# Performance work log

Measured on AMD Instinct MI355X. Metric: run time of the kernel, lower is better.

Reference implementation:

```python
import jax, jax.numpy as jnp
import numpy as np

LN_EPS = 1e-5
DEG_EPS = 1e-12


def setup_inputs() -> dict:
    key = jax.random.key(0)
    k1, k2, k3, k4 = jax.random.split(key, 4)
    N, E, D = 100000, 1000000, 64
    x = jax.random.normal(k1, (N, D), dtype=jnp.float32)
    edge_index = jax.random.randint(k2, (2, E), 0, N, dtype=jnp.int64)
    edge_weight = jax.random.uniform(k3, (E,), dtype=jnp.float32)
    # xavier_uniform for Linear(D, D): bound = sqrt(6/(D+D))
    bound = float(np.sqrt(6.0 / (D + D)))
    W = jax.random.uniform(k4, (D, D), dtype=jnp.float32, minval=-bound, maxval=bound)
    b = jnp.zeros((D,), dtype=jnp.float32)
    ln_gamma = jnp.ones((D,), dtype=jnp.float32)
    ln_beta = jnp.zeros((D,), dtype=jnp.float32)
    return {"x": x, "edge_index": edge_index, "edge_weight": edge_weight,
            "W": W, "b": b, "ln_gamma": ln_gamma, "ln_beta": ln_beta}


def reference(x, edge_index, edge_weight, W, b, ln_gamma, ln_beta):
    N = x.shape[0]
    # --- add self loops with weight 1.0 ---
    diag = jnp.arange(N, dtype=edge_index.dtype)
    ei = jnp.concatenate([edge_index, jnp.stack([diag, diag], axis=0)], axis=1)
    ew = jnp.concatenate([edge_weight.astype(jnp.float32),
                          jnp.ones((N,), dtype=jnp.float32)], axis=0)
    row, col = ei[0], ei[1]
    # --- renormalized adjacency weights: D^{-1/2}(A+I)D^{-1/2} ---
    deg = jax.ops.segment_sum(ew, row, num_segments=N)  # [N]
    deg_inv_sqrt = (deg + DEG_EPS) ** -0.5
    nw = ew * deg_inv_sqrt[row] * deg_inv_sqrt[col]     # [E+N]
    # --- SpMM: gather, scale, segment-sum ---
    msg = x[col] * nw[:, None].astype(x.dtype)          # [E+N, D]
    h = jax.ops.segment_sum(msg, row, num_segments=N)   # [N, D]
    # --- linear + gelu (exact erf) + layernorm + residual ---
    y = h @ W.T + b
    y = jax.nn.gelu(y, approximate=False)
    mean = jnp.mean(y, axis=-1, keepdims=True)
    var = jnp.mean(jnp.square(y - mean), axis=-1, keepdims=True)
    y = (y - mean) * jax.lax.rsqrt(var + LN_EPS) * ln_gamma + ln_beta
    return y + x
```

## Files before the change

kernel.cpp:

```cpp
#include <hip/hip_runtime.h>
#include <math.h>

#define DEG_EPS 1e-12f
#define LN_EPS  1e-5f
#define BROWS   128
#define CAPA    1536
#define MAXBKT  1024
#define CHUNK   2048

typedef __attribute__((ext_vector_type(8))) short bf16x8;
typedef __attribute__((ext_vector_type(4))) float f32x4;

__device__ __forceinline__ short f2bf(float f) {
    unsigned u = __float_as_uint(f);
    u += 0x7FFF + ((u >> 16) & 1);
    return (short)(u >> 16);
}
__device__ __forceinline__ float bf_lo(unsigned u) { return __uint_as_float(u << 16); }
__device__ __forceinline__ float bf_hi(unsigned u) { return __uint_as_float(u & 0xFFFF0000u); }


__global__ __launch_bounds__(256) void k_prep(
    const int* __restrict__ rows, const int* __restrict__ cols,
    const float* __restrict__ ew,
    int* __restrict__ bktcnt, int2* __restrict__ bktbuf,
    const float* __restrict__ x, const float* __restrict__ W,
    unsigned short* __restrict__ xwb,
    int E, int N, int NBKT, int Ntiles, int cB)
{
    const int t = threadIdx.x;
    if ((int)blockIdx.x < cB) {
        __shared__ int hist[MAXBKT];
        __shared__ int base_s[MAXBKT];
        __shared__ int cur[MAXBKT];
        __shared__ int srow[CHUNK];
        const int e0 = blockIdx.x * CHUNK;
        const int tc = min(E - e0, CHUNK);

        for (int i = t; i < NBKT; i += 256) { hist[i] = 0; cur[i] = 0; }
        __syncthreads();
        for (int i = t; i < tc; i += 256) {
            int r = rows[e0 + i];
            srow[i] = r;
            atomicAdd(&hist[r >> 7], 1);
        }
        __syncthreads();
        for (int i = t; i < NBKT; i += 256) {
            int h = hist[i];
            base_s[i] = h ? atomicAdd(&bktcnt[i], h) : 0;
        }
        __syncthreads();
        for (int i = t; i < tc; i += 256) {
            int r = srow[i];
            int bkt = r >> 7;
            int slot = base_s[bkt] + atomicAdd(&cur[bkt], 1);
            if (slot < CAPA)
                bktbuf[(size_t)bkt * CAPA + slot] =
                    make_int2(((r & 127) << 17) | cols[e0 + i],
                              __float_as_int(ew[e0 + i]));
        }
    } else {
        const int lane = t & 63;
        const int m = lane & 15;
        const int q = lane >> 4;
        const int xwB = gridDim.x - cB;
        const int wave = (blockIdx.x - cB) * 4 + (t >> 6);
        const int nwv = xwB * 4;

        bf16x8 bfrag[4][2];
#pragma unroll
        for (int f = 0; f < 4; ++f)
#pragma unroll
            for (int s = 0; s < 2; ++s) {
                const float4* wp = (const float4*)(W + (f * 16 + m) * 64 + s * 32 + q * 8);
                float4 lo = wp[0], hi = wp[1];
                bf16x8 v;
                v[0] = f2bf(lo.x); v[1] = f2bf(lo.y); v[2] = f2bf(lo.z); v[3] = f2bf(lo.w);
                v[4] = f2bf(hi.x); v[5] = f2bf(hi.y); v[6] = f2bf(hi.z); v[7] = f2bf(hi.w);
                bfrag[f][s] = v;
            }

        for (int tt = wave; tt < Ntiles; tt += nwv) {
            int n0 = tt * 16;
            int nr = n0 + m; if (nr >= N) nr = N - 1;
            bf16x8 afrag[2];
#pragma unroll
            for (int s = 0; s < 2; ++s) {
                const float4* xp = (const float4*)(x + (size_t)nr * 64 + s * 32 + q * 8);
                float4 lo = xp[0], hi = xp[1];
                bf16x8 v;
                v[0] = f2bf(lo.x); v[1] = f2bf(lo.y); v[2] = f2bf(lo.z); v[3] = f2bf(lo.w);
                v[4] = f2bf(hi.x); v[5] = f2bf(hi.y); v[6] = f2bf(hi.z); v[7] = f2bf(hi.w);
                afrag[s] = v;
            }
#pragma unroll
            for (int f = 0; f < 4; ++f) {
                f32x4 acc = {0.f, 0.f, 0.f, 0.f};
                acc = __builtin_amdgcn_mfma_f32_16x16x32_bf16(afrag[0], bfrag[f][0], acc, 0, 0, 0);
                acc = __builtin_amdgcn_mfma_f32_16x16x32_bf16(afrag[1], bfrag[f][1], acc, 0, 0, 0);
#pragma unroll
                for (int r4 = 0; r4 < 4; ++r4) {
                    int node = n0 + q * 4 + r4;
                    if (node < N)
                        xwb[(size_t)node * 64 + f * 16 + m] = (unsigned short)f2bf(acc[r4]);
                }
            }
        }
    }
}

__global__ __launch_bounds__(256) void k_dis(
    const int* __restrict__ bktcnt, const int2* __restrict__ bktbuf,
    float* __restrict__ dis, int N)
{
    __shared__ unsigned lsum[BROWS];
    const int bkt = blockIdx.x, t = threadIdx.x;
    if (t < BROWS) lsum[t] = 0;
    __syncthreads();
    int nb = bktcnt[bkt];
    if (nb > CAPA) nb = CAPA;
    const int2* buf = bktbuf + (size_t)bkt * CAPA;
    for (int i = t; i < nb; i += 256) {
        int2 e = buf[i];
        atomicAdd(&lsum[(e.x >> 17) & 127],
                  __float2uint_rn(__int_as_float(e.y) * 16777216.0f));
    }
    __syncthreads();
    int r = bkt * BROWS + t;
    if (t < BROWS && r < N) {
        float deg = 1.0f + (float)lsum[t] * (1.0f / 16777216.0f);
        dis[r] = rsqrtf(deg + DEG_EPS);
    }
}

__global__ __launch_bounds__(512) void k_spmm_fused(
    const int* __restrict__ bktcnt, const int2* __restrict__ bktbuf,
    const float* __restrict__ dis, const uint2* __restrict__ xw4,
    const float* __restrict__ x, const float* __restrict__ bias,
    const float* __restrict__ gamma, const float* __restrict__ beta,
    float* __restrict__ out, int N)
{
    __shared__ int2  srt[CAPA];
    __shared__ int   cnt[BROWS], off[BROWS], cur[BROWS], sc[BROWS];
    __shared__ float sdis[BROWS];
    const int t = threadIdx.x;
    const int bkt = blockIdx.x;
    const int r0 = bkt * BROWS;

    if (t < BROWS) {
        cnt[t] = 0; cur[t] = 0;
        sdis[t] = (r0 + t < N) ? dis[r0 + t] : 1.0f;
    }
    __syncthreads();

    int nb = bktcnt[bkt];
    if (nb > CAPA) nb = CAPA;
    const int2* buf = bktbuf + (size_t)bkt * CAPA;

    int2 eb[3];
#pragma unroll
    for (int u = 0; u < 3; ++u) {
        int i = t + u * 512;
        eb[u] = (i < nb) ? buf[i] : make_int2(-1, 0);
    }
#pragma unroll
    for (int u = 0; u < 3; ++u)
        if (eb[u].x >= 0)
            atomicAdd(&cnt[(eb[u].x >> 17) & 127], 1);
    __syncthreads();

    int v = 0;
    if (t < BROWS) { v = cnt[t]; sc[t] = v; }
    __syncthreads();
    for (int o = 1; o < BROWS; o <<= 1) {
        int u2 = 0;
        if (t < BROWS && t >= o) u2 = sc[t - o];
        __syncthreads();
        if (t < BROWS) sc[t] += u2;
        __syncthreads();
    }
    if (t < BROWS) off[t] = sc[t] - v;
    __syncthreads();

#pragma unroll
    for (int u = 0; u < 3; ++u)
        if (eb[u].x >= 0) {
            int rl = (eb[u].x >> 17) & 127;
            int c  = eb[u].x & 0x1FFFF;
            float w = __int_as_float(eb[u].y) * sdis[rl] * dis[c];
            int pos = off[rl] + atomicAdd(&cur[rl], 1);
            srt[pos] = make_int2(c, __float_as_int(w));
        }
    __syncthreads();

    const int lane = t & 63, wv = t >> 6;
    const int k  = lane & 15;
    const int qh = lane >> 4;

    for (int i = 0; i < 16; ++i) {
        const int rl = wv * 16 + i;
        const int row = r0 + rl;
        if (row >= N) break;

        int rcnt = cnt[rl]; if (rcnt > 64) rcnt = 64;
        int rbase = off[rl];
        float s = sdis[rl];

        float a0 = 0.f, a1 = 0.f, a2 = 0.f, a3 = 0.f;
        if (qh == 0) {
            float s2 = s * s;
            uint2 vv = xw4[(size_t)row * 16 + k];
            a0 = bf_lo(vv.x) * s2; a1 = bf_hi(vv.x) * s2;
            a2 = bf_lo(vv.y) * s2; a3 = bf_hi(vv.y) * s2;
        }

        int c = 0; float w = 0.f;
        if (lane < rcnt) {
            int2 m = srt[rbase + lane];
            c = m.x;
            w = __int_as_float(m.y);
        }

        int tmax = (rcnt + 3) >> 2;
        int tt = 0;
        for (; tt + 2 <= tmax; tt += 2) {
            int j0 = 4 * tt + qh, j1 = j0 + 4;
            int   c0 = __shfl(c, j0, 64);
            float w0 = __shfl(w, j0, 64);
            int   c1 = __shfl(c, j1, 64);
            float w1 = __shfl(w, j1, 64);
            uint2 v0 = xw4[(size_t)c0 * 16 + k];
            uint2 v1 = xw4[(size_t)c1 * 16 + k];
            a0 = fmaf(bf_lo(v0.x), w0, a0); a1 = fmaf(bf_hi(v0.x), w0, a1);
            a2 = fmaf(bf_lo(v0.y), w0, a2); a3 = fmaf(bf_hi(v0.y), w0, a3);
            a0 = fmaf(bf_lo(v1.x), w1, a0); a1 = fmaf(bf_hi(v1.x), w1, a1);
            a2 = fmaf(bf_lo(v1.y), w1, a2); a3 = fmaf(bf_hi(v1.y), w1, a3);
        }
        if (tt < tmax) {
            int j = 4 * tt + qh;
            int   cc = __shfl(c, j, 64);
            float ww = __shfl(w, j, 64);
            uint2 vv = xw4[(size_t)cc * 16 + k];
            a0 = fmaf(bf_lo(vv.x), ww, a0); a1 = fmaf(bf_hi(vv.x), ww, a1);
            a2 = fmaf(bf_lo(vv.y), ww, a2); a3 = fmaf(bf_hi(vv.y), ww, a3);
        }

#pragma unroll
        for (int mk = 16; mk < 64; mk <<= 1) {
            a0 += __shfl_xor(a0, mk, 64);
            a1 += __shfl_xor(a1, mk, 64);
            a2 += __shfl_xor(a2, mk, 64);
            a3 += __shfl_xor(a3, mk, 64);
        }

        float a = (qh == 0) ? a0 : (qh == 1) ? a1 : (qh == 2) ? a2 : a3;
        int f = 4 * k + qh;
        a += bias[f];
        a = 0.5f * a * (1.0f + erff(a * 0.70710678118654752f));

        float sum = a, ssq = a * a;
#pragma unroll
        for (int mk = 1; mk < 64; mk <<= 1) {
            sum += __shfl_xor(sum, mk, 64);
            ssq += __shfl_xor(ssq, mk, 64);
        }
        float mean = sum * (1.0f / 64.0f);
        float var  = fmaxf(ssq * (1.0f / 64.0f) - mean * mean, 0.0f);
        float rs   = rsqrtf(var + LN_EPS);
        float nrm  = (a - mean) * rs;

        float nv = __shfl(nrm, ((lane & 3) << 4) | (lane >> 2), 64);
        out[(size_t)row * 64 + lane] =
            nv * gamma[lane] + beta[lane] + x[(size_t)row * 64 + lane];
    }
}

extern "C" void kernel_launch(void* const* d_in, const int* in_sizes, int n_in,
                              void* d_out, int out_size, void* d_ws, size_t ws_size,
                              hipStream_t stream) {
    const float* x   = (const float*)d_in[0];
    const int*   ei  = (const int*)  d_in[1];
    const float* ew  = (const float*)d_in[2];
    const float* W   = (const float*)d_in[3];
    const float* b   = (const float*)d_in[4];
    const float* g   = (const float*)d_in[5];
    const float* bt  = (const float*)d_in[6];
    float* out = (float*)d_out;

    const int N = in_sizes[0] / 64;
    const int E = in_sizes[1] / 2;
    const int* rows = ei;
    const int* cols = ei + E;
    const int Ntiles = (N + 15) / 16;
    const int NBKT = (N + BROWS - 1) / BROWS;

    char* w8 = (char*)d_ws;
    int2*  bktbuf = (int2*)w8;                    w8 += (size_t)NBKT * CAPA * 8;
    unsigned short* xwb = (unsigned short*)w8;    w8 += (size_t)N * 128;
    float* dis    = (float*)w8;                   w8 += (size_t)N * 4;
    int*   bktcnt = (int*)w8;

    hipMemsetAsync(bktcnt, 0, (size_t)NBKT * 4, stream);

    const int cB = (E + CHUNK - 1) / CHUNK;
    const int xB = 1024;
    k_prep<<<cB + xB, 256, 0, stream>>>(rows, cols, ew, bktcnt, bktbuf,
                                        x, W, xwb, E, N, NBKT, Ntiles, cB);

    k_dis<<<NBKT, 256, 0, stream>>>(bktcnt, bktbuf, dis, N);

    k_spmm_fused<<<NBKT, 512, 0, stream>>>(
        bktcnt, bktbuf, dis, (const uint2*)xwb, x, b, g, bt, out, N);
}
```

Measured before the change: 178.0 us.

## Fold degree computation into prep via global atomics and split SpMM blocks by half-bucket

Removes the separate degree kernel: k_prep now accumulates fixed-point degrees with global atomicAdd per edge, and the SpMM kernel computes rsqrt degree on the fly. The SpMM kernel is relaunched with two 256-thread blocks per 128-row bucket, each handling 64 rows and filtering the bucket's edges, which reduces shared memory and raises block count. The cost is a million global atomics in prep, each half-block reading the whole bucket buffer (double edge reads), and an extra rsqrt per edge.

```diff
diff --git a/kernel.cpp b/kernel.cpp
--- a/kernel.cpp
+++ b/kernel.cpp
@@ -7,6 +7,7 @@
 #define CAPA    1536
 #define MAXBKT  1024
 #define CHUNK   2048
+#define SCAP    896
 
 typedef __attribute__((ext_vector_type(8))) short bf16x8;
 typedef __attribute__((ext_vector_type(4))) float f32x4;
@@ -18,12 +19,16 @@
 }
 __device__ __forceinline__ float bf_lo(unsigned u) { return __uint_as_float(u << 16); }
 __device__ __forceinline__ float bf_hi(unsigned u) { return __uint_as_float(u & 0xFFFF0000u); }
+__device__ __forceinline__ float deg2dis(unsigned fx) {
+    return rsqrtf(1.0f + (float)fx * (1.0f / 16777216.0f) + DEG_EPS);
+}
 
 
 __global__ __launch_bounds__(256) void k_prep(
     const int* __restrict__ rows, const int* __restrict__ cols,
     const float* __restrict__ ew,
     int* __restrict__ bktcnt, int2* __restrict__ bktbuf,
+    unsigned* __restrict__ deg,
     const float* __restrict__ x, const float* __restrict__ W,
     unsigned short* __restrict__ xwb,
     int E, int N, int NBKT, int Ntiles, int cB)
@@ -53,11 +58,12 @@
         for (int i = t; i < tc; i += 256) {
             int r = srow[i];
             int bkt = r >> 7;
+            float we = ew[e0 + i];
+            atomicAdd(&deg[r], __float2uint_rn(we * 16777216.0f));
             int slot = base_s[bkt] + atomicAdd(&cur[bkt], 1);
             if (slot < CAPA)
                 bktbuf[(size_t)bkt * CAPA + slot] =
-                    make_int2(((r & 127) << 17) | cols[e0 + i],
-                              __float_as_int(ew[e0 + i]));
+                    make_int2(((r & 127) << 17) | cols[e0 + i], __float_as_int(we));
         }
     } else {
         const int lane = t & 63;
@@ -109,47 +115,25 @@
     }
 }
 
-__global__ __launch_bounds__(256) void k_dis(
+__global__ __launch_bounds__(256) void k_spmm_fused(
     const int* __restrict__ bktcnt, const int2* __restrict__ bktbuf,
-    float* __restrict__ dis, int N)
-{
-    __shared__ unsigned lsum[BROWS];
-    const int bkt = blockIdx.x, t = threadIdx.x;
-    if (t < BROWS) lsum[t] = 0;
-    __syncthreads();
-    int nb = bktcnt[bkt];
-    if (nb > CAPA) nb = CAPA;
-    const int2* buf = bktbuf + (size_t)bkt * CAPA;
-    for (int i = t; i < nb; i += 256) {
-        int2 e = buf[i];
-        atomicAdd(&lsum[(e.x >> 17) & 127],
-                  __float2uint_rn(__int_as_float(e.y) * 16777216.0f));
-    }
-    __syncthreads();
-    int r = bkt * BROWS + t;
-    if (t < BROWS && r < N) {
-        float deg = 1.0f + (float)lsum[t] * (1.0f / 16777216.0f);
-        dis[r] = rsqrtf(deg + DEG_EPS);
-    }
-}
-
-__global__ __launch_bounds__(512) void k_spmm_fused(
-    const int* __restrict__ bktcnt, const int2* __restrict__ bktbuf,
-    const float* __restrict__ dis, const uint2* __restrict__ xw4,
+    const unsigned* __restrict__ deg, const uint2* __restrict__ xw4,
     const float* __restrict__ x, const float* __restrict__ bias,
     const float* __restrict__ gamma, const float* __restrict__ beta,
     float* __restrict__ out, int N)
 {
-    __shared__ int2  srt[CAPA];
-    __shared__ int   cnt[BROWS], off[BROWS], cur[BROWS], sc[BROWS];
-    __shared__ float sdis[BROWS];
+    __shared__ int2  srt[SCAP];
+    __shared__ int   cnt[64], off[64], cur[64], sc[64];
+    __shared__ float sdis[64];
     const int t = threadIdx.x;
-    const int bkt = blockIdx.x;
-    const int r0 = bkt * BROWS;
-
-    if (t < BROWS) {
+    const int bkt  = blockIdx.x >> 1;
+    const int half = blockIdx.x & 1;
+    const int r0 = bkt * BROWS + half * 64;
+
+    if (t < 64) {
         cnt[t] = 0; cur[t] = 0;
-        sdis[t] = (r0 + t < N) ? dis[r0 + t] : 1.0f;
+        int r = r0 + t;
+        sdis[t] = (r < N) ? deg2dis(deg[r]) : 1.0f;
     }
     __syncthreads();
 
@@ -157,39 +141,43 @@
     if (nb > CAPA) nb = CAPA;
     const int2* buf = bktbuf + (size_t)bkt * CAPA;
 
-    int2 eb[3];
-#pragma unroll
-    for (int u = 0; u < 3; ++u) {
-        int i = t + u * 512;
+    int2 eb[6];
+#pragma unroll
+    for (int u = 0; u < 6; ++u) {
+        int i = t + u * 256;
         eb[u] = (i < nb) ? buf[i] : make_int2(-1, 0);
     }
 #pragma unroll
-    for (int u = 0; u < 3; ++u)
-        if (eb[u].x >= 0)
-            atomicAdd(&cnt[(eb[u].x >> 17) & 127], 1);
+    for (int u = 0; u < 6; ++u)
+        if (eb[u].x >= 0) {
+            int rq = (eb[u].x >> 17) & 127;
+            if ((rq >> 6) != half) eb[u].x = -1;
+            else atomicAdd(&cnt[rq & 63], 1);
+        }
     __syncthreads();
 
     int v = 0;
-    if (t < BROWS) { v = cnt[t]; sc[t] = v; }
-    __syncthreads();
-    for (int o = 1; o < BROWS; o <<= 1) {
+    if (t < 64) { v = cnt[t]; sc[t] = v; }
+    __syncthreads();
+    for (int o = 1; o < 64; o <<= 1) {
         int u2 = 0;
-        if (t < BROWS && t >= o) u2 = sc[t - o];
-        __syncthreads();
-        if (t < BROWS) sc[t] += u2;
-        __syncthreads();
-    }
-    if (t < BROWS) off[t] = sc[t] - v;
-    __syncthreads();
-
-#pragma unroll
-    for (int u = 0; u < 3; ++u)
+        if (t < 64 && t >= o) u2 = sc[t - o];
+        __syncthreads();
+        if (t < 64) sc[t] += u2;
+        __syncthreads();
+    }
+    if (t < 64) off[t] = sc[t] - v;
+    __syncthreads();
+
+#pragma unroll
+    for (int u = 0; u < 6; ++u)
         if (eb[u].x >= 0) {
-            int rl = (eb[u].x >> 17) & 127;
+            int rl = (eb[u].x >> 17) & 63;
             int c  = eb[u].x & 0x1FFFF;
-            float w = __int_as_float(eb[u].y) * sdis[rl] * dis[c];
+            float w = __int_as_float(eb[u].y) * sdis[rl] * deg2dis(deg[c]);
             int pos = off[rl] + atomicAdd(&cur[rl], 1);
-            srt[pos] = make_int2(c, __float_as_int(w));
+            if (pos < SCAP)
+                srt[pos] = make_int2(c, __float_as_int(w));
         }
     __syncthreads();
 
@@ -297,18 +285,17 @@
     char* w8 = (char*)d_ws;
     int2*  bktbuf = (int2*)w8;                    w8 += (size_t)NBKT * CAPA * 8;
     unsigned short* xwb = (unsigned short*)w8;    w8 += (size_t)N * 128;
-    float* dis    = (float*)w8;                   w8 += (size_t)N * 4;
+    unsigned* deg = (unsigned*)w8;                w8 += (size_t)N * 4;
     int*   bktcnt = (int*)w8;
 
-    hipMemsetAsync(bktcnt, 0, (size_t)NBKT * 4, stream);
+    hipMemsetAsync(deg, 0, (size_t)N * 4 + (size_t)NBKT * 4, stream);
 
     const int cB = (E + CHUNK - 1) / CHUNK;
     const int xB = 1024;
-    k_prep<<<cB + xB, 256, 0, stream>>>(rows, cols, ew, bktcnt, bktbuf,
+    k_prep<<<cB + xB, 256, 0, stream>>>(rows, cols, ew, bktcnt, bktbuf, deg,
                                         x, W, xwb, E, N, NBKT, Ntiles, cB);
 
-    k_dis<<<NBKT, 256, 0, stream>>>(bktcnt, bktbuf, dis, N);
-
-    k_spmm_fused<<<NBKT, 512, 0, stream>>>(
-        bktcnt, bktbuf, dis, (const uint2*)xwb, x, b, g, bt, out, N);
-}
+    const int spmmB = (N + 63) / 64;
+    k_spmm_fused<<<spmmB, 256, 0, stream>>>(
+        bktcnt, bktbuf, deg, (const uint2*)xwb, x, b, g, bt, out, N);
+}
```

After: 201.1 us. +13.0%, slower.
